# Kernel optimization log

Measured on AMD Instinct MI355X. Metric: run time of the kernel, lower is better.

The kernel has to match this reference:

```python
import jax, jax.numpy as jnp
import numpy as np

EMBED = 1024
HEADS = 16
HEAD_SIZE = EMBED // HEADS
B, T = 2, 2048
EPS = 1e-5


def layer_norm(x, g, b):
    mu = jnp.mean(x, axis=-1, keepdims=True)
    var = jnp.var(x, axis=-1, keepdims=True)
    return (x - mu) * jax.lax.rsqrt(var + EPS) * g + b


def setup_inputs() -> dict:
    key = jax.random.key(0)
    ks = jax.random.split(key, 12)
    s = 0.02
    return {
        "x": jax.random.normal(ks[0], (B, T, EMBED), jnp.float32),
        "Wq": s * jax.random.normal(ks[1], (EMBED, EMBED), jnp.float32),
        "Wk": s * jax.random.normal(ks[2], (EMBED, EMBED), jnp.float32),
        "Wv": s * jax.random.normal(ks[3], (EMBED, EMBED), jnp.float32),
        "Wo": s * jax.random.normal(ks[4], (EMBED, EMBED), jnp.float32),
        "bo": jnp.zeros((EMBED,), jnp.float32),
        "W1": s * jax.random.normal(ks[5], (EMBED, 4 * EMBED), jnp.float32),
        "b1": jnp.zeros((4 * EMBED,), jnp.float32),
        "W2": s * jax.random.normal(ks[6], (4 * EMBED, EMBED), jnp.float32),
        "b2": jnp.zeros((EMBED,), jnp.float32),
        "ln1_g": jnp.ones((EMBED,), jnp.float32),
        "ln1_b": jnp.zeros((EMBED,), jnp.float32),
        "ln2_g": jnp.ones((EMBED,), jnp.float32),
        "ln2_b": jnp.zeros((EMBED,), jnp.float32),
    }


def reference(x, Wq, Wk, Wv, Wo, bo, W1, b1, W2, b2, ln1_g, ln1_b, ln2_g, ln2_b):
    # --- multi-head causal self-attention on ln1(x) ---
    h = layer_norm(x, ln1_g, ln1_b)                      # [B,T,D]
    q = (h @ Wq).reshape(B, T, HEADS, HEAD_SIZE)         # per-head Q (concat layout)
    k = (h @ Wk).reshape(B, T, HEADS, HEAD_SIZE)
    v = (h @ Wv).reshape(B, T, HEADS, HEAD_SIZE)
    scores = jnp.einsum("bqhd,bkhd->bhqk", q, k) / jnp.sqrt(
        jnp.asarray(HEAD_SIZE, x.dtype)
    )                                                    # [B,H,T,T]
    causal = jnp.tril(jnp.ones((T, T), bool))
    scores = jnp.where(causal, scores, -jnp.inf)
    wei = jax.nn.softmax(scores, axis=-1)
    attn = jnp.einsum("bhqk,bkhd->bqhd", wei, v).reshape(B, T, EMBED)
    x = x + attn @ Wo + bo                               # residual (dropout=0)
    # --- feed-forward on ln2(x) ---
    h2 = layer_norm(x, ln2_g, ln2_b)
    ff = jax.nn.relu(h2 @ W1 + b1) @ W2 + b2
    return x + ff
```

## Files before the change

### kernel.cpp

```cpp
#include <hip/hip_runtime.h>


typedef __bf16 bf16;
typedef __attribute__((ext_vector_type(8))) __bf16 bf16x8;
typedef __attribute__((ext_vector_type(4))) __bf16 bf16x4;
typedef __attribute__((ext_vector_type(4))) short  shortx4;
typedef __attribute__((ext_vector_type(4))) float  floatx4;

__device__ __forceinline__ short f2bf_bits(float x) {
  return __builtin_bit_cast(short, (bf16)x);
}

__device__ __forceinline__ void gl2lds16(const bf16* g, bf16* l) {
  __builtin_amdgcn_global_load_lds((const __attribute__((address_space(1))) void*)g,
                                   (__attribute__((address_space(3))) void*)l, 16, 0, 0);
}

__global__ __launch_bounds__(256) void prep_kernel(
    const float* __restrict__ Wq, const float* __restrict__ Wk,
    const float* __restrict__ Wv, const float* __restrict__ Wo,
    const float* __restrict__ W1, const float* __restrict__ W2,
    bf16* __restrict__ WqkvT, bf16* __restrict__ WoT,
    bf16* __restrict__ W1T, bf16* __restrict__ W2T,
    const float* __restrict__ x, const float* __restrict__ ln1g,
    const float* __restrict__ ln1b, bf16* __restrict__ h1)
{
  int id = blockIdx.x;
  if (id >= 12288) {
    const int row = id - 12288, t = threadIdx.x;
    const float* xr = x + (size_t)row * 1024;
    float4 v = *(const float4*)(xr + t * 4);
    float s  = v.x + v.y + v.z + v.w;
    float s2 = v.x * v.x + v.y * v.y + v.z * v.z + v.w * v.w;
    #pragma unroll
    for (int off = 1; off < 64; off <<= 1) {
      s  += __shfl_xor(s, off);
      s2 += __shfl_xor(s2, off);
    }
    __shared__ float ps[4], ps2[4];
    int wv = t >> 6;
    if ((t & 63) == 0) { ps[wv] = s; ps2[wv] = s2; }
    __syncthreads();
    s  = ps[0] + ps[1] + ps[2] + ps[3];
    s2 = ps2[0] + ps2[1] + ps2[2] + ps2[3];
    const float mu = s * (1.0f / 1024.0f);
    const float rstd = rsqrtf(s2 * (1.0f / 1024.0f) - mu * mu + 1e-5f);
    float4 gv = *(const float4*)(ln1g + t * 4);
    float4 bv = *(const float4*)(ln1b + t * 4);
    bf16x4 o;
    o[0] = (bf16)((v.x - mu) * rstd * gv.x + bv.x);
    o[1] = (bf16)((v.y - mu) * rstd * gv.y + bv.y);
    o[2] = (bf16)((v.z - mu) * rstd * gv.z + bv.z);
    o[3] = (bf16)((v.w - mu) * rstd * gv.w + bv.w);
    *(bf16x4*)(h1 + (size_t)row * 1024 + t * 4) = o;
    return;
  }
  const float* src; bf16* dst; int K, N, tile;
  if (id < 4096) {
    K = 1024; N = 1024; tile = id & 1023;
    int wsel = id >> 10;
    src = (wsel == 0) ? Wq : (wsel == 1) ? Wk : (wsel == 2) ? Wv : Wo;
    dst = (wsel < 3) ? (WqkvT + (size_t)wsel * 1024 * 1024) : WoT;
  } else if (id < 8192) {
    K = 1024; N = 4096; tile = id - 4096; src = W1; dst = W1T;
  } else {
    K = 4096; N = 1024; tile = id - 8192; src = W2; dst = W2T;
  }
  int ntn = N >> 5;
  int k0 = (tile / ntn) * 32, n0 = (tile % ntn) * 32;
  __shared__ float tl[32][33];
  int tr = threadIdx.x >> 3, tc = (threadIdx.x & 7) * 4;
  float4 v = *(const float4*)(src + (size_t)(k0 + tr) * N + n0 + tc);
  tl[tr][tc + 0] = v.x; tl[tr][tc + 1] = v.y; tl[tr][tc + 2] = v.z; tl[tr][tc + 3] = v.w;
  __syncthreads();
  bf16x4 o = { (bf16)tl[tc + 0][tr], (bf16)tl[tc + 1][tr],
               (bf16)tl[tc + 2][tr], (bf16)tl[tc + 3][tr] };
  *(bf16x4*)(dst + (size_t)(n0 + tr) * K + k0 + tc) = o;
}

__device__ __forceinline__ void gemm_core(
    const bf16* __restrict__ A, const bf16* __restrict__ Bt,
    int Ktot, int k0, int k1, bf16* As, bf16* Bs, floatx4 (&acc)[4][4])
{
  const int tid = threadIdx.x, lane = tid & 63, wv = tid >> 6;
  const int li = lane & 15, g = lane >> 4;
  const int wm = wv >> 1, wn = wv & 1;
  const int srow = wv * 16 + (lane >> 2);
  const int scol = (lane & 3) * 8;
  const bf16* aP = A  + (size_t)srow * Ktot + scol;
  const bf16* bP = Bt + (size_t)srow * Ktot + scol;
  bf16* AsW = As + wv * 512;
  bf16* BsW = Bs + wv * 512;
  for (int kt = k0; kt < k1; kt += 64) {
    gl2lds16(aP + kt,                          AsW);
    gl2lds16(aP + kt + (size_t)64 * Ktot,      AsW + 2048);
    gl2lds16(aP + kt + 32,                     AsW + 4096);
    gl2lds16(aP + kt + 32 + (size_t)64 * Ktot, AsW + 6144);
    gl2lds16(bP + kt,                          BsW);
    gl2lds16(bP + kt + (size_t)64 * Ktot,      BsW + 2048);
    gl2lds16(bP + kt + 32,                     BsW + 4096);
    gl2lds16(bP + kt + 32 + (size_t)64 * Ktot, BsW + 6144);
    __syncthreads();
    #pragma unroll
    for (int hh = 0; hh < 2; ++hh) {
      const bf16* Ap = As + hh * 4096;
      const bf16* Bp = Bs + hh * 4096;
      bf16x8 af[4], bfr[4];
      #pragma unroll
      for (int r = 0; r < 4; ++r)
        af[r] = *(const bf16x8*)(Ap + (wm * 64 + r * 16 + li) * 32 + g * 8);
      #pragma unroll
      for (int c = 0; c < 4; ++c)
        bfr[c] = *(const bf16x8*)(Bp + (wn * 64 + c * 16 + li) * 32 + g * 8);
      #pragma unroll
      for (int r = 0; r < 4; ++r)
        #pragma unroll
        for (int c = 0; c < 4; ++c)
          acc[r][c] = __builtin_amdgcn_mfma_f32_16x16x32_bf16(bfr[c], af[r], acc[r][c], 0, 0, 0);
    }
    __syncthreads();
  }
}

template<bool BIAS, bool RELU, bool RESID>
__global__ __launch_bounds__(256) void gemm_kernel(
    const bf16* __restrict__ A, const bf16* __restrict__ Bt,
    const float* __restrict__ bias, const float* __restrict__ resid,
    bf16* __restrict__ Cb, float* __restrict__ Cf,
    int M, int N, int K)
{
  __shared__ bf16 As[8192];
  __shared__ bf16 Bs[8192];
  const int lane = threadIdx.x & 63, wv = threadIdx.x >> 6;
  const int li = lane & 15, g = lane >> 4;
  const int m0 = blockIdx.x * 128, n0 = blockIdx.y * 128;
  const int wm = wv >> 1, wn = wv & 1;
  floatx4 acc[4][4] = {};
  gemm_core(A + (size_t)m0 * K, Bt + (size_t)n0 * K, K, 0, K, As, Bs, acc);
  #pragma unroll
  for (int r = 0; r < 4; ++r) {
    int rowC = m0 + wm * 64 + r * 16 + li;
    #pragma unroll
    for (int c = 0; c < 4; ++c) {
      int colC = n0 + wn * 64 + c * 16 + g * 4;
      float4 bv = BIAS ? *(const float4*)(bias + colC) : float4{0, 0, 0, 0};
      float v0 = acc[r][c][0] + bv.x, v1 = acc[r][c][1] + bv.y;
      float v2 = acc[r][c][2] + bv.z, v3 = acc[r][c][3] + bv.w;
      if (RELU) {
        v0 = fmaxf(v0, 0.f); v1 = fmaxf(v1, 0.f);
        v2 = fmaxf(v2, 0.f); v3 = fmaxf(v3, 0.f);
      }
      size_t idx = (size_t)rowC * N + colC;
      if (RESID) {
        float4 rv = *(const float4*)(resid + idx);
        float4 ov = { v0 + rv.x, v1 + rv.y, v2 + rv.z, v3 + rv.w };
        *(float4*)(Cf + idx) = ov;
      } else {
        bf16x4 ov = { (bf16)v0, (bf16)v1, (bf16)v2, (bf16)v3 };
        *(bf16x4*)(Cb + idx) = ov;
      }
    }
  }
}

__global__ __launch_bounds__(256) void gemm_qkv(
    const bf16* __restrict__ A, const bf16* __restrict__ Bt,
    bf16* __restrict__ qkv, bf16* __restrict__ VtG)
{
  const int K = 1024;
  __shared__ bf16 As[8192];
  __shared__ bf16 Bs[8192];
  const int lane = threadIdx.x & 63, wv = threadIdx.x >> 6;
  const int li = lane & 15, g = lane >> 4;
  const int m0 = blockIdx.x * 128, n0 = blockIdx.y * 128;
  const int wm = wv >> 1, wn = wv & 1;
  floatx4 acc[4][4] = {};
  gemm_core(A + (size_t)m0 * K, Bt + (size_t)n0 * K, K, 0, K, As, Bs, acc);
  if (n0 < 2048) {
    #pragma unroll
    for (int r = 0; r < 4; ++r) {
      int rowC = m0 + wm * 64 + r * 16 + li;
      #pragma unroll
      for (int c = 0; c < 4; ++c) {
        int colC = n0 + wn * 64 + c * 16 + g * 4;
        bf16x4 ov = { (bf16)acc[r][c][0], (bf16)acc[r][c][1],
                      (bf16)acc[r][c][2], (bf16)acc[r][c][3] };
        *(bf16x4*)(qkv + (size_t)rowC * 3072 + colC) = ov;
      }
    }
  } else {
    #pragma unroll
    for (int r = 0; r < 4; ++r) {
      int rowC = m0 + wm * 64 + r * 16 + li;
      int key = rowC & 2047, bq = rowC >> 11;
      #pragma unroll
      for (int c = 0; c < 4; ++c) {
        int vcol0 = n0 + wn * 64 + c * 16 + g * 4 - 2048;
        #pragma unroll
        for (int e = 0; e < 4; ++e) {
          int vcol = vcol0 + e;
          int hh = vcol >> 6, d = vcol & 63;
          VtG[((size_t)(bq * 16 + hh) * 64 + d) * 2048 + key] = (bf16)acc[r][c][e];
        }
      }
    }
  }
}

__global__ __launch_bounds__(256) void gemm_splitk(
    const bf16* __restrict__ A, const bf16* __restrict__ Bt,
    bf16* __restrict__ Cp, int M, int N, int Ktot, int Kc)
{
  __shared__ bf16 As[8192];
  __shared__ bf16 Bs[8192];
  const int lane = threadIdx.x & 63, wv = threadIdx.x >> 6;
  const int li = lane & 15, g = lane >> 4;
  const int m0 = blockIdx.x * 128, n0 = blockIdx.y * 128;
  const int z = blockIdx.z;
  const int wm = wv >> 1, wn = wv & 1;
  floatx4 acc[4][4] = {};
  gemm_core(A + (size_t)m0 * Ktot, Bt + (size_t)n0 * Ktot, Ktot,
            z * Kc, (z + 1) * Kc, As, Bs, acc);
  bf16* C = Cp + (size_t)z * M * N;
  #pragma unroll
  for (int r = 0; r < 4; ++r) {
    int rowC = m0 + wm * 64 + r * 16 + li;
    #pragma unroll
    for (int c = 0; c < 4; ++c) {
      int colC = n0 + wn * 64 + c * 16 + g * 4;
      bf16x4 ov = { (bf16)acc[r][c][0], (bf16)acc[r][c][1],
                    (bf16)acc[r][c][2], (bf16)acc[r][c][3] };
      *(bf16x4*)(C + (size_t)rowC * N + colC) = ov;
    }
  }
}

__global__ __launch_bounds__(256) void combine_wo_ln2(
    const bf16* __restrict__ P, const float* __restrict__ bo,
    const float* __restrict__ x, const float* __restrict__ gam,
    const float* __restrict__ bet, float* __restrict__ x2, bf16* __restrict__ h2)
{
  const int row = blockIdx.x, t = threadIdx.x;
  const size_t base = (size_t)row * 1024 + t * 4;
  float4 v = *(const float4*)(x + base);
  bf16x4 p0 = *(const bf16x4*)(P + base);
  bf16x4 p1 = *(const bf16x4*)(P + 4194304 + base);
  float4 bv = *(const float4*)(bo + t * 4);
  v.x += (float)p0[0] + (float)p1[0] + bv.x;
  v.y += (float)p0[1] + (float)p1[1] + bv.y;
  v.z += (float)p0[2] + (float)p1[2] + bv.z;
  v.w += (float)p0[3] + (float)p1[3] + bv.w;
  *(float4*)(x2 + base) = v;
  float s  = v.x + v.y + v.z + v.w;
  float s2 = v.x * v.x + v.y * v.y + v.z * v.z + v.w * v.w;
  #pragma unroll
  for (int off = 1; off < 64; off <<= 1) {
    s  += __shfl_xor(s, off);
    s2 += __shfl_xor(s2, off);
  }
  __shared__ float ps[4], ps2[4];
  int wv = t >> 6;
  if ((t & 63) == 0) { ps[wv] = s; ps2[wv] = s2; }
  __syncthreads();
  s  = ps[0] + ps[1] + ps[2] + ps[3];
  s2 = ps2[0] + ps2[1] + ps2[2] + ps2[3];
  const float mu = s * (1.0f / 1024.0f);
  const float rstd = rsqrtf(s2 * (1.0f / 1024.0f) - mu * mu + 1e-5f);
  float4 gv = *(const float4*)(gam + t * 4);
  float4 bb = *(const float4*)(bet + t * 4);
  bf16x4 o;
  o[0] = (bf16)((v.x - mu) * rstd * gv.x + bb.x);
  o[1] = (bf16)((v.y - mu) * rstd * gv.y + bb.y);
  o[2] = (bf16)((v.z - mu) * rstd * gv.z + bb.z);
  o[3] = (bf16)((v.w - mu) * rstd * gv.w + bb.w);
  *(bf16x4*)(h2 + base) = o;
}

__global__ __launch_bounds__(256) void combine_ffn2(
    const bf16* __restrict__ P, const float* __restrict__ b2,
    const float* __restrict__ x2, float* __restrict__ out)
{
  const size_t i = ((size_t)blockIdx.x * 256 + threadIdx.x) * 4;
  const int col = (int)(i & 1023);
  float4 acc = *(const float4*)(x2 + i);
  float4 bv = *(const float4*)(b2 + col);
  acc.x += bv.x; acc.y += bv.y; acc.z += bv.z; acc.w += bv.w;
  #pragma unroll
  for (int z = 0; z < 4; ++z) {
    bf16x4 p = *(const bf16x4*)(P + (size_t)z * 4194304 + i);
    acc.x += (float)p[0]; acc.y += (float)p[1];
    acc.z += (float)p[2]; acc.w += (float)p[3];
  }
  *(float4*)(out + i) = acc;
}

__global__ __launch_bounds__(256, 2) void attn_kernel(
    const bf16* __restrict__ qkv, const bf16* __restrict__ VtG,
    bf16* __restrict__ attnb)
{
  __shared__ bf16 Ks[2][64 * 72];
  __shared__ bf16 Vt[2][64 * 72];
  const int t = threadIdx.x, lane = t & 63, wv = t >> 6;
  const int li = lane & 15, g = lane >> 4;
  const int p = blockIdx.x & 15, h = (blockIdx.x >> 4) & 15, b = blockIdx.x >> 8;
  const int row0 = b << 11;
  const int tlo = p * 4 + wv, thi = 127 - tlo;
  const int q0l = tlo << 4, q0h = thi << 4;
  const size_t qkvbase = (size_t)row0 * 3072 + (size_t)h * 64;
  const bf16* vgbase = VtG + (size_t)(b * 16 + h) * 64 * 2048;

  const bf16* qpl = qkv + qkvbase + (size_t)(q0l + li) * 3072 + g * 8;
  const bf16* qph = qkv + qkvbase + (size_t)(q0h + li) * 3072 + g * 8;
  bf16x8 bl0 = *(const bf16x8*)(qpl), bl1 = *(const bf16x8*)(qpl + 32);
  bf16x8 bh0 = *(const bf16x8*)(qph), bh1 = *(const bf16x8*)(qph + 32);

  floatx4 ol[4] = {}, oh[4] = {};
  float ll = 0.f, lh = 0.f;
  const int cmax = 31 - p;

  const int krow0 = t >> 3, kdc = (t & 7) * 8;
  const int vd = t >> 2, vkg = (t & 3) * 16;
  bf16x8 kv0, kv1, vv0, vv1;

  auto ld = [&](int c) {
    const size_t kb = qkvbase + (size_t)(c * 64) * 3072 + 1024;
    kv0 = *(const bf16x8*)(qkv + kb + (size_t)krow0 * 3072 + kdc);
    kv1 = *(const bf16x8*)(qkv + kb + (size_t)(krow0 + 32) * 3072 + kdc);
    const bf16* vg = vgbase + (size_t)vd * 2048 + c * 64 + vkg;
    vv0 = *(const bf16x8*)(vg);
    vv1 = *(const bf16x8*)(vg + 8);
  };
  auto wr = [&](int buf) {
    *(bf16x8*)(Ks[buf] + krow0 * 72 + kdc)        = kv0;
    *(bf16x8*)(Ks[buf] + (krow0 + 32) * 72 + kdc) = kv1;
    *(bf16x8*)(Vt[buf] + vd * 72 + vkg)           = vv0;
    *(bf16x8*)(Vt[buf] + vd * 72 + vkg + 8)       = vv1;
  };

  auto proc = [&](const bf16* KsB, const bf16* VtB,
                  const bf16x8& bq0, const bf16x8& bq1, float& l_i,
                  floatx4 (&o)[4], int qg, int k0, bool diag) {
    floatx4 sv[4];
    #pragma unroll
    for (int s = 0; s < 4; ++s) {
      const bf16* kr = KsB + (s * 16 + li) * 72 + g * 8;
      bf16x8 a0 = *(const bf16x8*)(kr);
      bf16x8 a1 = *(const bf16x8*)(kr + 32);
      floatx4 z = {0.f, 0.f, 0.f, 0.f};
      z = __builtin_amdgcn_mfma_f32_16x16x32_bf16(a0, bq0, z, 0, 0, 0);
      z = __builtin_amdgcn_mfma_f32_16x16x32_bf16(a1, bq1, z, 0, 0, 0);
      sv[s] = z;
    }
    float pv[4][4];
    float rs = 0.f;
    #pragma unroll
    for (int s = 0; s < 4; ++s)
      #pragma unroll
      for (int e = 0; e < 4; ++e) {
        float val = __expf(sv[s][e] * 0.125f - 4.0f);
        if (diag) {
          int kg = k0 + s * 16 + g * 4 + e;
          val = (kg <= qg) ? val : 0.0f;
        }
        pv[s][e] = val;
        rs += val;
      }
    rs += __shfl_xor(rs, 16);
    rs += __shfl_xor(rs, 32);
    l_i += rs;
    #pragma unroll
    for (int s = 0; s < 4; ++s) {
      shortx4 bp = { f2bf_bits(pv[s][0]), f2bf_bits(pv[s][1]),
                     f2bf_bits(pv[s][2]), f2bf_bits(pv[s][3]) };
      #pragma unroll
      for (int c = 0; c < 4; ++c) {
        shortx4 av = *(const shortx4*)(VtB + (c * 16 + li) * 72 + s * 16 + g * 4);
        o[c] = __builtin_amdgcn_mfma_f32_16x16x16bf16_1k(av, bp, o[c], 0, 0, 0);
      }
    }
  };

  ld(0);
  wr(0);
  __syncthreads();
  int buf = 0;
  for (int c = 0; c <= cmax; ++c) {
    if (c < cmax) ld(c + 1);
    proc(Ks[buf], Vt[buf], bh0, bh1, lh, oh, q0h + li, c * 64, c == cmax);
    if (c <= p) proc(Ks[buf], Vt[buf], bl0, bl1, ll, ol, q0l + li, c * 64, c == p);
    if (c < cmax) wr(buf ^ 1);
    __syncthreads();
    buf ^= 1;
  }

  const float invh = 1.0f / lh, invl = 1.0f / ll;
  #pragma unroll
  for (int c = 0; c < 4; ++c) {
    bf16x4 ovh = { (bf16)(oh[c][0] * invh), (bf16)(oh[c][1] * invh),
                   (bf16)(oh[c][2] * invh), (bf16)(oh[c][3] * invh) };
    *(bf16x4*)(attnb + (size_t)(row0 + q0h + li) * 1024 + h * 64 + c * 16 + g * 4) = ovh;
    bf16x4 ovl = { (bf16)(ol[c][0] * invl), (bf16)(ol[c][1] * invl),
                   (bf16)(ol[c][2] * invl), (bf16)(ol[c][3] * invl) };
    *(bf16x4*)(attnb + (size_t)(row0 + q0l + li) * 1024 + h * 64 + c * 16 + g * 4) = ovl;
  }
}

extern "C" void kernel_launch(void* const* d_in, const int* in_sizes, int n_in,
                              void* d_out, int out_size, void* d_ws, size_t ws_size,
                              hipStream_t stream) {
  (void)in_sizes; (void)n_in; (void)out_size; (void)ws_size;
  const float* x    = (const float*)d_in[0];
  const float* Wq   = (const float*)d_in[1];
  const float* Wk   = (const float*)d_in[2];
  const float* Wv   = (const float*)d_in[3];
  const float* Wo   = (const float*)d_in[4];
  const float* bo   = (const float*)d_in[5];
  const float* W1   = (const float*)d_in[6];
  const float* b1   = (const float*)d_in[7];
  const float* W2   = (const float*)d_in[8];
  const float* b2   = (const float*)d_in[9];
  const float* ln1g = (const float*)d_in[10];
  const float* ln1b = (const float*)d_in[11];
  const float* ln2g = (const float*)d_in[12];
  const float* ln2b = (const float*)d_in[13];
  float* out = (float*)d_out;
  char* ws = (char*)d_ws;

  constexpr size_t OFF_WQKVT = 0;
  constexpr size_t OFF_WOT   = OFF_WQKVT + 3072ull * 1024 * 2;
  constexpr size_t OFF_W1T   = OFF_WOT   + 1024ull * 1024 * 2;
  constexpr size_t OFF_W2T   = OFF_W1T   + 4096ull * 1024 * 2;
  constexpr size_t OFF_H1    = OFF_W2T   + 1024ull * 4096 * 2;
  constexpr size_t OFF_QKV   = OFF_H1    + 4096ull * 1024 * 2;
  constexpr size_t OFF_ATT   = OFF_QKV   + 4096ull * 3072 * 2;
  constexpr size_t OFF_X2    = OFF_ATT   + 4096ull * 1024 * 2;
  constexpr size_t OFF_H2    = OFF_X2    + 4096ull * 1024 * 4;
  constexpr size_t OFF_F1    = OFF_H2    + 4096ull * 1024 * 2;
  constexpr size_t OFF_PART  = OFF_F1    + 4096ull * 4096 * 2;
  constexpr size_t OFF_VTG   = OFF_PART  + 4ull * 4096 * 1024 * 2;

  bf16*  WqkvT = (bf16*)(ws + OFF_WQKVT);
  bf16*  WoT   = (bf16*)(ws + OFF_WOT);
  bf16*  W1T   = (bf16*)(ws + OFF_W1T);
  bf16*  W2T   = (bf16*)(ws + OFF_W2T);
  bf16*  h1    = (bf16*)(ws + OFF_H1);
  bf16*  qkv   = (bf16*)(ws + OFF_QKV);
  bf16*  attnb = (bf16*)(ws + OFF_ATT);
  float* x2    = (float*)(ws + OFF_X2);
  bf16*  h2    = (bf16*)(ws + OFF_H2);
  bf16*  f1    = (bf16*)(ws + OFF_F1);
  bf16*  part  = (bf16*)(ws + OFF_PART);
  bf16*  vtg   = (bf16*)(ws + OFF_VTG);

  prep_kernel<<<16384, 256, 0, stream>>>(Wq, Wk, Wv, Wo, W1, W2,
                                         WqkvT, WoT, W1T, W2T, x, ln1g, ln1b, h1);
  gemm_qkv<<<dim3(32, 24), 256, 0, stream>>>(h1, WqkvT, qkv, vtg);
  attn_kernel<<<512, 256, 0, stream>>>(qkv, vtg, attnb);
  gemm_splitk<<<dim3(32, 8, 2), 256, 0, stream>>>(attnb, WoT, part, 4096, 1024, 1024, 512);
  combine_wo_ln2<<<4096, 256, 0, stream>>>(part, bo, x, ln2g, ln2b, x2, h2);
  gemm_kernel<true, true, false><<<dim3(32, 32), 256, 0, stream>>>(
      h2, W1T, b1, nullptr, f1, nullptr, 4096, 4096, 1024);
  gemm_splitk<<<dim3(32, 8, 4), 256, 0, stream>>>(f1, W2T, part, 4096, 1024, 4096, 1024);
  combine_ffn2<<<4096, 256, 0, stream>>>(part, b2, x2, out);
}
```

Measured before the change: 350.0 us.

## Use 256x256 eight-wave GEMM tiles with ping-pong LDS pipeline

```diff
diff --git a/kernel.cpp b/kernel.cpp
--- a/kernel.cpp
+++ b/kernel.cpp
@@ -14,6 +14,12 @@
 __device__ __forceinline__ void gl2lds16(const bf16* g, bf16* l) {
   __builtin_amdgcn_global_load_lds((const __attribute__((address_space(1))) void*)g,
                                    (__attribute__((address_space(3))) void*)l, 16, 0, 0);
+}
+
+__device__ __forceinline__ void barx() {
+  asm volatile("" ::: "memory");
+  __builtin_amdgcn_s_barrier();
+  asm volatile("" ::: "memory");
 }
 
 __global__ __launch_bounds__(256) void prep_kernel(
@@ -122,91 +128,6 @@
   }
 }
 
-template<bool BIAS, bool RELU, bool RESID>
-__global__ __launch_bounds__(256) void gemm_kernel(
-    const bf16* __restrict__ A, const bf16* __restrict__ Bt,
-    const float* __restrict__ bias, const float* __restrict__ resid,
-    bf16* __restrict__ Cb, float* __restrict__ Cf,
-    int M, int N, int K)
-{
-  __shared__ bf16 As[8192];
-  __shared__ bf16 Bs[8192];
-  const int lane = threadIdx.x & 63, wv = threadIdx.x >> 6;
-  const int li = lane & 15, g = lane >> 4;
-  const int m0 = blockIdx.x * 128, n0 = blockIdx.y * 128;
-  const int wm = wv >> 1, wn = wv & 1;
-  floatx4 acc[4][4] = {};
-  gemm_core(A + (size_t)m0 * K, Bt + (size_t)n0 * K, K, 0, K, As, Bs, acc);
-  #pragma unroll
-  for (int r = 0; r < 4; ++r) {
-    int rowC = m0 + wm * 64 + r * 16 + li;
-    #pragma unroll
-    for (int c = 0; c < 4; ++c) {
-      int colC = n0 + wn * 64 + c * 16 + g * 4;
-      float4 bv = BIAS ? *(const float4*)(bias + colC) : float4{0, 0, 0, 0};
-      float v0 = acc[r][c][0] + bv.x, v1 = acc[r][c][1] + bv.y;
-      float v2 = acc[r][c][2] + bv.z, v3 = acc[r][c][3] + bv.w;
-      if (RELU) {
-        v0 = fmaxf(v0, 0.f); v1 = fmaxf(v1, 0.f);
-        v2 = fmaxf(v2, 0.f); v3 = fmaxf(v3, 0.f);
-      }
-      size_t idx = (size_t)rowC * N + colC;
-      if (RESID) {
-        float4 rv = *(const float4*)(resid + idx);
-        float4 ov = { v0 + rv.x, v1 + rv.y, v2 + rv.z, v3 + rv.w };
-        *(float4*)(Cf + idx) = ov;
-      } else {
-        bf16x4 ov = { (bf16)v0, (bf16)v1, (bf16)v2, (bf16)v3 };
-        *(bf16x4*)(Cb + idx) = ov;
-      }
-    }
-  }
-}
-
-__global__ __launch_bounds__(256) void gemm_qkv(
-    const bf16* __restrict__ A, const bf16* __restrict__ Bt,
-    bf16* __restrict__ qkv, bf16* __restrict__ VtG)
-{
-  const int K = 1024;
-  __shared__ bf16 As[8192];
-  __shared__ bf16 Bs[8192];
-  const int lane = threadIdx.x & 63, wv = threadIdx.x >> 6;
-  const int li = lane & 15, g = lane >> 4;
-  const int m0 = blockIdx.x * 128, n0 = blockIdx.y * 128;
-  const int wm = wv >> 1, wn = wv & 1;
-  floatx4 acc[4][4] = {};
-  gemm_core(A + (size_t)m0 * K, Bt + (size_t)n0 * K, K, 0, K, As, Bs, acc);
-  if (n0 < 2048) {
-    #pragma unroll
-    for (int r = 0; r < 4; ++r) {
-      int rowC = m0 + wm * 64 + r * 16 + li;
-      #pragma unroll
-      for (int c = 0; c < 4; ++c) {
-        int colC = n0 + wn * 64 + c * 16 + g * 4;
-        bf16x4 ov = { (bf16)acc[r][c][0], (bf16)acc[r][c][1],
-                      (bf16)acc[r][c][2], (bf16)acc[r][c][3] };
-        *(bf16x4*)(qkv + (size_t)rowC * 3072 + colC) = ov;
-      }
-    }
-  } else {
-    #pragma unroll
-    for (int r = 0; r < 4; ++r) {
-      int rowC = m0 + wm * 64 + r * 16 + li;
-      int key = rowC & 2047, bq = rowC >> 11;
-      #pragma unroll
-      for (int c = 0; c < 4; ++c) {
-        int vcol0 = n0 + wn * 64 + c * 16 + g * 4 - 2048;
-        #pragma unroll
-        for (int e = 0; e < 4; ++e) {
-          int vcol = vcol0 + e;
-          int hh = vcol >> 6, d = vcol & 63;
-          VtG[((size_t)(bq * 16 + hh) * 64 + d) * 2048 + key] = (bf16)acc[r][c][e];
-        }
-      }
-    }
-  }
-}
-
 __global__ __launch_bounds__(256) void gemm_splitk(
     const bf16* __restrict__ A, const bf16* __restrict__ Bt,
     bf16* __restrict__ Cp, int M, int N, int Ktot, int Kc)
@@ -230,6 +151,202 @@
       int colC = n0 + wn * 64 + c * 16 + g * 4;
       bf16x4 ov = { (bf16)acc[r][c][0], (bf16)acc[r][c][1],
                     (bf16)acc[r][c][2], (bf16)acc[r][c][3] };
+      *(bf16x4*)(C + (size_t)rowC * N + colC) = ov;
+    }
+  }
+}
+
+
+#define MFMA_PHASE(RH, CH, BB)                                                  \
+  do {                                                                          \
+    __builtin_amdgcn_s_setprio(1);                                              \
+    _Pragma("unroll") for (int ks = 0; ks < 2; ++ks)                            \
+      _Pragma("unroll") for (int r = 0; r < 4; ++r)                             \
+        _Pragma("unroll") for (int c = 0; c < 2; ++c)                           \
+          acc[(RH) * 4 + r][(CH) * 2 + c] =                                     \
+            __builtin_amdgcn_mfma_f32_16x16x32_bf16(                            \
+                BB[c][ks], af[r][ks], acc[(RH) * 4 + r][(CH) * 2 + c], 0, 0, 0);\
+    __builtin_amdgcn_s_setprio(0);                                              \
+  } while (0)
+
+__device__ __forceinline__ void gemm8_core(
+    const bf16* __restrict__ A, const bf16* __restrict__ Bt,
+    int K, int k0, int k1, bf16* lds, floatx4 (&acc)[8][4])
+{
+  const int lane = threadIdx.x & 63, wv = threadIdx.x >> 6;
+  const int li = lane & 15, g = lane >> 4;
+  const int wm2 = wv >> 2, wn4 = wv & 3;
+  const int nt = (k1 - k0) >> 6;
+
+  const int srow  = wv * 16 + (lane >> 3);
+  const int schnk = ((lane & 7) ^ (lane >> 3)) * 8;
+  const bf16* aSrc = A  + (size_t)srow * K + k0 + schnk;
+  const bf16* bSrc = Bt + (size_t)srow * K + k0 + schnk;
+  const size_t row8 = (size_t)8 * K;
+  bf16* ldsB = lds + 32768;
+
+  const int xk0 = ((0 + g) ^ (li & 7)) * 8;
+  const int xk1 = ((4 + g) ^ (li & 7)) * 8;
+
+  auto stA = [&](int t, int h) {
+    if (t < nt) {
+      const bf16* gp = aSrc + (size_t)(h * 128) * K + (t << 6);
+      bf16* lp = lds + (((t & 1) * 2 + h) << 13) + wv * 1024;
+      gl2lds16(gp, lp);
+      gl2lds16(gp + row8, lp + 512);
+    }
+  };
+  auto stB = [&](int t, int h) {
+    if (t < nt) {
+      const bf16* gp = bSrc + (size_t)(h * 128) * K + (t << 6);
+      bf16* lp = ldsB + (((t & 1) * 2 + h) << 13) + wv * 1024;
+      gl2lds16(gp, lp);
+      gl2lds16(gp + row8, lp + 512);
+    }
+  };
+
+  bf16x8 af[4][2], bA[2][2], bB[2][2];
+  auto ldA = [&](int b, int RH) {
+    const bf16* base = lds + ((b * 2 + RH) << 13) + (wm2 * 64 + li) * 64;
+    #pragma unroll
+    for (int r = 0; r < 4; ++r) {
+      af[r][0] = *(const bf16x8*)(base + r * 1024 + xk0);
+      af[r][1] = *(const bf16x8*)(base + r * 1024 + xk1);
+    }
+  };
+  auto ldB = [&](int b, int CH, bf16x8 (&bb)[2][2]) {
+    const bf16* base = ldsB + ((b * 2 + CH) << 13) + (wn4 * 32 + li) * 64;
+    #pragma unroll
+    for (int c = 0; c < 2; ++c) {
+      bb[c][0] = *(const bf16x8*)(base + c * 1024 + xk0);
+      bb[c][1] = *(const bf16x8*)(base + c * 1024 + xk1);
+    }
+  };
+
+  stA(0, 0); stB(0, 0); stB(0, 1); stA(0, 1);
+  stA(1, 0); stB(1, 0);
+  asm volatile("s_waitcnt vmcnt(4)" ::: "memory");
+  barx();
+
+  for (int t = 0; t < nt; ++t) {
+    const int b = t & 1;
+    ldA(b, 0); ldB(b, 0, bA);
+    stB(t + 1, 1);
+    barx();
+    MFMA_PHASE(0, 0, bA);
+    barx();
+    ldB(b, 1, bB);
+    stA(t + 1, 1);
+    asm volatile("s_waitcnt vmcnt(8)" ::: "memory");
+    barx();
+    MFMA_PHASE(0, 1, bB);
+    barx();
+    ldA(b, 1);
+    stA(t + 2, 0);
+    barx();
+    MFMA_PHASE(1, 0, bA);
+    barx();
+    stB(t + 2, 0);
+    asm volatile("s_waitcnt vmcnt(6)" ::: "memory");
+    barx();
+    MFMA_PHASE(1, 1, bB);
+    barx();
+  }
+}
+
+__global__ __launch_bounds__(512, 2) void gemm8_ffn1(
+    const bf16* __restrict__ A, const bf16* __restrict__ Bt,
+    const float* __restrict__ bias, bf16* __restrict__ C,
+    int M, int N, int K)
+{
+  __shared__ bf16 lds8[65536];
+  const int m0 = blockIdx.x * 256, n0 = blockIdx.y * 256;
+  floatx4 acc[8][4] = {};
+  gemm8_core(A + (size_t)m0 * K, Bt + (size_t)n0 * K, K, 0, K, lds8, acc);
+  const int lane = threadIdx.x & 63, wv = threadIdx.x >> 6;
+  const int li = lane & 15, g = lane >> 4;
+  const int wm2 = wv >> 2, wn4 = wv & 3;
+  #pragma unroll
+  for (int ar = 0; ar < 8; ++ar) {
+    int rowC = m0 + (ar >> 2) * 128 + wm2 * 64 + (ar & 3) * 16 + li;
+    #pragma unroll
+    for (int ac = 0; ac < 4; ++ac) {
+      int colC = n0 + (ac >> 1) * 128 + wn4 * 32 + (ac & 1) * 16 + g * 4;
+      float4 bv = *(const float4*)(bias + colC);
+      bf16x4 ov = { (bf16)fmaxf(acc[ar][ac][0] + bv.x, 0.f),
+                    (bf16)fmaxf(acc[ar][ac][1] + bv.y, 0.f),
+                    (bf16)fmaxf(acc[ar][ac][2] + bv.z, 0.f),
+                    (bf16)fmaxf(acc[ar][ac][3] + bv.w, 0.f) };
+      *(bf16x4*)(C + (size_t)rowC * N + colC) = ov;
+    }
+  }
+}
+
+__global__ __launch_bounds__(512, 2) void gemm8_qkv(
+    const bf16* __restrict__ A, const bf16* __restrict__ Bt,
+    bf16* __restrict__ qkv, bf16* __restrict__ VtG)
+{
+  const int K = 1024;
+  __shared__ bf16 lds8[65536];
+  const int m0 = blockIdx.x * 256, n0 = blockIdx.y * 256;
+  floatx4 acc[8][4] = {};
+  gemm8_core(A + (size_t)m0 * K, Bt + (size_t)n0 * K, K, 0, K, lds8, acc);
+  const int lane = threadIdx.x & 63, wv = threadIdx.x >> 6;
+  const int li = lane & 15, g = lane >> 4;
+  const int wm2 = wv >> 2, wn4 = wv & 3;
+  if (n0 < 2048) {
+    #pragma unroll
+    for (int ar = 0; ar < 8; ++ar) {
+      int rowC = m0 + (ar >> 2) * 128 + wm2 * 64 + (ar & 3) * 16 + li;
+      #pragma unroll
+      for (int ac = 0; ac < 4; ++ac) {
+        int colC = n0 + (ac >> 1) * 128 + wn4 * 32 + (ac & 1) * 16 + g * 4;
+        bf16x4 ov = { (bf16)acc[ar][ac][0], (bf16)acc[ar][ac][1],
+                      (bf16)acc[ar][ac][2], (bf16)acc[ar][ac][3] };
+        *(bf16x4*)(qkv + (size_t)rowC * 3072 + colC) = ov;
+      }
+    }
+  } else {
+    #pragma unroll
+    for (int ar = 0; ar < 8; ++ar) {
+      int rowC = m0 + (ar >> 2) * 128 + wm2 * 64 + (ar & 3) * 16 + li;
+      int key = rowC & 2047, bq = rowC >> 11;
+      #pragma unroll
+      for (int ac = 0; ac < 4; ++ac) {
+        int vcol0 = n0 + (ac >> 1) * 128 + wn4 * 32 + (ac & 1) * 16 + g * 4 - 2048;
+        #pragma unroll
+        for (int e = 0; e < 4; ++e) {
+          int vcol = vcol0 + e;
+          int hh = vcol >> 6, d = vcol & 63;
+          VtG[((size_t)(bq * 16 + hh) * 64 + d) * 2048 + key] = (bf16)acc[ar][ac][e];
+        }
+      }
+    }
+  }
+}
+
+__global__ __launch_bounds__(512, 2) void gemm8_splitk(
+    const bf16* __restrict__ A, const bf16* __restrict__ Bt,
+    bf16* __restrict__ Cp, int M, int N, int Ktot, int Kc)
+{
+  __shared__ bf16 lds8[65536];
+  const int m0 = blockIdx.x * 256, n0 = blockIdx.y * 256;
+  const int z = blockIdx.z;
+  floatx4 acc[8][4] = {};
+  gemm8_core(A + (size_t)m0 * Ktot, Bt + (size_t)n0 * Ktot, Ktot,
+             z * Kc, (z + 1) * Kc, lds8, acc);
+  const int lane = threadIdx.x & 63, wv = threadIdx.x >> 6;
+  const int li = lane & 15, g = lane >> 4;
+  const int wm2 = wv >> 2, wn4 = wv & 3;
+  bf16* C = Cp + (size_t)z * M * N;
+  #pragma unroll
+  for (int ar = 0; ar < 8; ++ar) {
+    int rowC = m0 + (ar >> 2) * 128 + wm2 * 64 + (ar & 3) * 16 + li;
+    #pragma unroll
+    for (int ac = 0; ac < 4; ++ac) {
+      int colC = n0 + (ac >> 1) * 128 + wn4 * 32 + (ac & 1) * 16 + g * 4;
+      bf16x4 ov = { (bf16)acc[ar][ac][0], (bf16)acc[ar][ac][1],
+                    (bf16)acc[ar][ac][2], (bf16)acc[ar][ac][3] };
       *(bf16x4*)(C + (size_t)rowC * N + colC) = ov;
     }
   }
@@ -454,12 +571,11 @@
 
   prep_kernel<<<16384, 256, 0, stream>>>(Wq, Wk, Wv, Wo, W1, W2,
                                          WqkvT, WoT, W1T, W2T, x, ln1g, ln1b, h1);
-  gemm_qkv<<<dim3(32, 24), 256, 0, stream>>>(h1, WqkvT, qkv, vtg);
+  gemm8_qkv<<<dim3(16, 12), 512, 0, stream>>>(h1, WqkvT, qkv, vtg);
   attn_kernel<<<512, 256, 0, stream>>>(qkv, vtg, attnb);
   gemm_splitk<<<dim3(32, 8, 2), 256, 0, stream>>>(attnb, WoT, part, 4096, 1024, 1024, 512);
   combine_wo_ln2<<<4096, 256, 0, stream>>>(part, bo, x, ln2g, ln2b, x2, h2);
-  gemm_kernel<true, true, false><<<dim3(32, 32), 256, 0, stream>>>(
-      h2, W1T, b1, nullptr, f1, nullptr, 4096, 4096, 1024);
-  gemm_splitk<<<dim3(32, 8, 4), 256, 0, stream>>>(f1, W2T, part, 4096, 1024, 4096, 1024);
+  gemm8_ffn1<<<dim3(16, 16), 512, 0, stream>>>(h2, W1T, b1, f1, 4096, 4096, 1024);
+  gemm8_splitk<<<dim3(16, 4, 4), 512, 0, stream>>>(f1, W2T, part, 4096, 1024, 4096, 1024);
   combine_ffn2<<<4096, 256, 0, stream>>>(part, b2, x2, out);
 }
```

After: 324.7 us. 1.08x faster.
